# Performance work log

Hardware: AMD Instinct MI355X
Metric: run time of the kernel (lower is better)

## Reference

```python
import jax, jax.numpy as jnp
import numpy as np
import math

EMBED = 8      # forced == n_qubits by the reshape in FeedForwardQuantum
HEADS = 4
DK = EMBED // HEADS
FFN = 2048
EPS = 1e-5


def _layer_norm(x, g, b):
    mu = jnp.mean(x, axis=-1, keepdims=True)
    var = jnp.mean((x - mu) ** 2, axis=-1, keepdims=True)
    return (x - mu) * jax.lax.rsqrt(var + EPS) * g + b


def setup_inputs() -> dict:
    key = jax.random.key(0)
    ks = jax.random.split(key, 8)
    B, S = 8, 2048
    s_e = 1.0 / math.sqrt(EMBED)
    s_q = 1.0 / math.sqrt(EMBED)   # linear1 fan_in = n_qubits = EMBED
    s_f = 1.0 / math.sqrt(FFN)
    return {
        "x": jax.random.normal(ks[0], (B, S, EMBED), dtype=jnp.float32),
        "Wp": jax.random.uniform(ks[1], (EMBED, EMBED), jnp.float32, -s_e, s_e),
        "Wo": jax.random.uniform(ks[2], (EMBED, EMBED), jnp.float32, -s_e, s_e),
        "g1": jnp.ones((EMBED,), jnp.float32),
        "b1": jnp.zeros((EMBED,), jnp.float32),
        "W1": jax.random.uniform(ks[3], (FFN, EMBED), jnp.float32, -s_q, s_q),
        "bb1": jax.random.uniform(ks[4], (FFN,), jnp.float32, -s_q, s_q),
        "W2": jax.random.uniform(ks[5], (EMBED, FFN), jnp.float32, -s_f, s_f),
        "bb2": jax.random.uniform(ks[6], (EMBED,), jnp.float32, -s_f, s_f),
        "g2": jnp.ones((EMBED,), jnp.float32),
        "b2": jnp.zeros((EMBED,), jnp.float32),
    }


def reference(x, Wp, Wo, g1, b1, W1, bb1, W2, bb2, g2, b2):
    B, S, E = x.shape
    # --- multi-head self-attention (q = k = v = proj(x)) ---
    proj = x @ Wp.T                                   # (B,S,E)
    qkv = proj.reshape(B, S, HEADS, DK).transpose(0, 2, 1, 3)  # (B,H,S,dk)
    scores = jnp.einsum("bhqd,bhkd->bhqk", qkv, qkv) / math.sqrt(DK)
    p = jax.nn.softmax(scores, axis=-1)               # (B,H,S,S)
    ctx = jnp.einsum("bhqk,bhkd->bhqd", p, qkv)
    merged = ctx.transpose(0, 2, 1, 3).reshape(B, S, E)
    attn_out = merged @ Wo.T
    x1 = _layer_norm(x + attn_out, g1, b1)
    # --- quantum FFN: RX per wire, CNOT ladder, Z-expectations ---
    # <Z_j> after the circuit = prod_{i<=j} cos(x_i)  (exact closed form)
    out_q = jnp.cumprod(jnp.cos(x1), axis=-1)         # (B,S,n_qubits==E)
    h = jax.nn.relu(out_q @ W1.T + bb1)               # (B,S,FFN)
    ffn_out = h @ W2.T + bb2                          # (B,S,E)
    return _layer_norm(x1 + ffn_out, g2, b2)
```

## Files before the change

kernel.cpp:

```cpp
#include <hip/hip_runtime.h>
#include <math.h>

#define NB   8
#define SEQ  2048
#define EMB  8
#define NH   4
#define NFF  2048
#define NTOK (NB*SEQ)
#define LNEPS 1e-5f

typedef float v2f __attribute__((ext_vector_type(2)));

__device__ __forceinline__ float fexp2(float x) {
#if __has_builtin(__builtin_amdgcn_exp2f)
    return __builtin_amdgcn_exp2f(x);
#else
    return exp2f(x);
#endif
}

__device__ __forceinline__ float dot8(const float4& a, const float4& b,
                                      const float4& c, const float4& d) {
    return a.x*b.x + a.y*b.y + a.z*b.z + a.w*b.w
         + c.x*d.x + c.y*d.y + c.z*d.z + c.w*d.w;
}

__global__ __launch_bounds__(128) void k_prep(const float* __restrict__ x,
                                              const float* __restrict__ Wp,
                                              const float* __restrict__ W2,
                                              float* __restrict__ projH,
                                              float* __restrict__ w2t) {
    int t = blockIdx.x * 128 + threadIdx.x;
    if (t < NTOK) {
        int b = t >> 11, s = t & (SEQ - 1);
        const float4* xr = (const float4*)(x + (size_t)t * EMB);
        float4 xa = xr[0], xb = xr[1];
        float o[8];
#pragma unroll
        for (int e = 0; e < 8; ++e) {
            const float4* wr = (const float4*)(Wp + e * EMB);
            o[e] = dot8(xa, wr[0], xb, wr[1]);
        }
#pragma unroll
        for (int h = 0; h < 4; ++h) {
            *(float2*)(projH + ((size_t)(b * 4 + h) * SEQ + s) * 2) =
                make_float2(o[2 * h], o[2 * h + 1]);
        }
    }
    if (t < NFF) {
        float o[8];
#pragma unroll
        for (int e = 0; e < 8; ++e) o[e] = W2[e * NFF + t];
        float4* wr = (float4*)(w2t + (size_t)t * EMB);
        wr[0] = make_float4(o[0], o[1], o[2], o[3]);
        wr[1] = make_float4(o[4], o[5], o[6], o[7]);
    }
}

#define QCA 64
__global__ __launch_bounds__(256) void k_attn(const float* __restrict__ projH,
                                              float* __restrict__ ctx) {
    __shared__ float Kx[SEQ];
    __shared__ float Ky[SEQ];
    __shared__ float red[3][8][QCA];

    int bid = blockIdx.x;
    int qc  = bid & 31;
    int bh  = bid >> 5;

    const float C   = 1.01001959058f;
    const float RC  = 0.99008003302f;
    const float4* gsr = (const float4*)(projH + (size_t)bh * SEQ * 2);
#pragma unroll
    for (int ii = 0; ii < 4; ++ii) {
        int i = threadIdx.x + 256 * ii;
        float4 v = gsr[i];
        *(float2*)&Kx[2 * i] = make_float2(v.x * C, v.z * C);
        *(float2*)&Ky[2 * i] = make_float2(v.y * C, v.w * C);
    }
    __syncthreads();

    int qg  = threadIdx.x & 31;
    int sub = threadIdx.x >> 5;

    int q0 = qc * QCA + qg * 2;
    float qxa = Kx[q0],     qya = Ky[q0];
    float qxb = Kx[q0 + 1], qyb = Ky[q0 + 1];
    v2f qx2a = {qxa, qxa}, qy2a = {qya, qya};
    v2f qx2b = {qxb, qxb}, qy2b = {qyb, qyb};

    v2f lA = {0.f, 0.f}, axA = {0.f, 0.f}, ayA = {0.f, 0.f};
    v2f lB = {0.f, 0.f}, axB = {0.f, 0.f}, ayB = {0.f, 0.f};

    const float4* Kx4 = (const float4*)Kx;
    const float4* Ky4 = (const float4*)Ky;
    int j04 = sub * 64;
#pragma unroll 2
    for (int jj = 0; jj < 64; ++jj) {
        float4 kx = Kx4[j04 + jj];
        float4 ky = Ky4[j04 + jj];
        v2f k0 = {kx.x, kx.y}, k1 = {kx.z, kx.w};
        v2f m0 = {ky.x, ky.y}, m1 = {ky.z, ky.w};

        v2f s0a = qx2a * k0 + qy2a * m0;
        v2f s1a = qx2a * k1 + qy2a * m1;
        v2f s0b = qx2b * k0 + qy2b * m0;
        v2f s1b = qx2b * k1 + qy2b * m1;

        v2f p0a, p1a, p0b, p1b;
        p0a.x = fexp2(s0a.x); p0a.y = fexp2(s0a.y);
        p1a.x = fexp2(s1a.x); p1a.y = fexp2(s1a.y);
        p0b.x = fexp2(s0b.x); p0b.y = fexp2(s0b.y);
        p1b.x = fexp2(s1b.x); p1b.y = fexp2(s1b.y);

        lA  += p0a;            lB  += p0b;
        axA += p0a * k0;       axB += p0b * k0;
        ayA += p0a * m0;       ayB += p0b * m0;
        lA  += p1a;            lB  += p1b;
        axA += p1a * k1;       axB += p1b * k1;
        ayA += p1a * m1;       ayB += p1b * m1;
    }
    red[0][sub][qg * 2]     = lA.x + lA.y;
    red[1][sub][qg * 2]     = axA.x + axA.y;
    red[2][sub][qg * 2]     = ayA.x + ayA.y;
    red[0][sub][qg * 2 + 1] = lB.x + lB.y;
    red[1][sub][qg * 2 + 1] = axB.x + axB.y;
    red[2][sub][qg * 2 + 1] = ayB.x + ayB.y;
    __syncthreads();

    if (threadIdx.x < QCA) {
        float L = 0.f, A0 = 0.f, A1 = 0.f;
#pragma unroll
        for (int s = 0; s < 8; ++s) {
            L  += red[0][s][threadIdx.x];
            A0 += red[1][s][threadIdx.x];
            A1 += red[2][s][threadIdx.x];
        }
        float inv = RC / L;
        int b = bh >> 2, h = bh & 3;
        int qglob = qc * QCA + threadIdx.x;
        *(float2*)(ctx + ((size_t)b * SEQ + qglob) * EMB + 2 * h) =
            make_float2(A0 * inv, A1 * inv);
    }
}

#define TB3  32
#define FCH3 32
__global__ __launch_bounds__(512) void k_ffn3(const float* __restrict__ ctx,
                                              const float* __restrict__ x,
                                              const float* __restrict__ Wo,
                                              const float* __restrict__ g1,
                                              const float* __restrict__ b1,
                                              const float* __restrict__ W1,
                                              const float* __restrict__ bb1,
                                              const float* __restrict__ w2t,
                                              const float* __restrict__ bb2,
                                              const float* __restrict__ g2,
                                              const float* __restrict__ b2,
                                              float* __restrict__ out) {
    __shared__ float q_lds[TB3][8];
    __shared__ float x1_lds[TB3][8];
    __shared__ float red[8][TB3][8];

    int tid = threadIdx.x;

    if (tid < TB3 * 8) {
        int tl = tid >> 3, e = tid & 7;
        int tok = blockIdx.x * TB3 + tl;
        const float4* cr = (const float4*)(ctx + (size_t)tok * EMB);
        float4 ca = cr[0], cb = cr[1];
        const float4* wr = (const float4*)(Wo + e * EMB);
        float ao = dot8(ca, wr[0], cb, wr[1]);
        float y = x[(size_t)tok * EMB + e] + ao;

        float s8 = y;
        s8 += __shfl_xor(s8, 1);
        s8 += __shfl_xor(s8, 2);
        s8 += __shfl_xor(s8, 4);
        float mu = s8 * 0.125f;
        float d  = y - mu;
        float vs = d * d;
        vs += __shfl_xor(vs, 1);
        vs += __shfl_xor(vs, 2);
        vs += __shfl_xor(vs, 4);
        float r = rsqrtf(vs * 0.125f + LNEPS);
        float v = d * r * g1[e] + b1[e];
        x1_lds[tl][e] = v;

        float p = __cosf(v);
        float t1 = __shfl_up(p, 1, 8); p = (e >= 1) ? p * t1 : p;
        float t2 = __shfl_up(p, 2, 8); p = (e >= 2) ? p * t2 : p;
        float t4 = __shfl_up(p, 4, 8); p = (e >= 4) ? p * t4 : p;
        q_lds[tl][e] = p;
    }
    __syncthreads();

    int tg  = tid & 7;
    int sub = tid >> 3;
    int tl0 = tg * 4;

    float4 qa[4], qb[4];
#pragma unroll
    for (int k = 0; k < 4; ++k) {
        qa[k] = *(const float4*)&q_lds[tl0 + k][0];
        qb[k] = *(const float4*)&q_lds[tl0 + k][4];
    }

    float acc[4][8];
#pragma unroll
    for (int k = 0; k < 4; ++k)
#pragma unroll
        for (int e = 0; e < 8; ++e) acc[k][e] = 0.f;

    int f0 = sub * FCH3;
#pragma unroll 4
    for (int i = 0; i < FCH3; ++i) {
        int f = f0 + i;
        const float4* w1r = (const float4*)(W1 + (size_t)f * EMB);
        float4 wa = w1r[0], wb = w1r[1];
        float bias = bb1[f];
        const float4* w2r = (const float4*)(w2t + (size_t)f * EMB);
        float4 va = w2r[0], vb = w2r[1];
#pragma unroll
        for (int k = 0; k < 4; ++k) {
            float hv = fmaxf(dot8(qa[k], wa, qb[k], wb) + bias, 0.f);
            acc[k][0] = fmaf(hv, va.x, acc[k][0]);
            acc[k][1] = fmaf(hv, va.y, acc[k][1]);
            acc[k][2] = fmaf(hv, va.z, acc[k][2]);
            acc[k][3] = fmaf(hv, va.w, acc[k][3]);
            acc[k][4] = fmaf(hv, vb.x, acc[k][4]);
            acc[k][5] = fmaf(hv, vb.y, acc[k][5]);
            acc[k][6] = fmaf(hv, vb.z, acc[k][6]);
            acc[k][7] = fmaf(hv, vb.w, acc[k][7]);
        }
    }

#pragma unroll
    for (int k = 0; k < 4; ++k)
#pragma unroll
        for (int e = 0; e < 8; ++e) {
            float v = acc[k][e];
            v += __shfl_xor(v, 8);
            v += __shfl_xor(v, 16);
            v += __shfl_xor(v, 32);
            acc[k][e] = v;
        }
    int wv = tid >> 6;
    if (((tid >> 3) & 7) == 0) {
#pragma unroll
        for (int k = 0; k < 4; ++k) {
            float4* d0 = (float4*)&red[wv][tl0 + k][0];
            d0[0] = make_float4(acc[k][0], acc[k][1], acc[k][2], acc[k][3]);
            d0[1] = make_float4(acc[k][4], acc[k][5], acc[k][6], acc[k][7]);
        }
    }
    __syncthreads();

    if (tid < TB3 * 8) {
        int rtok = tid >> 3, re = tid & 7;
        float v = 0.f;
#pragma unroll
        for (int w = 0; w < 8; ++w) v += red[w][rtok][re];
        int tok = blockIdx.x * TB3 + rtok;
        v += bb2[re] + x1_lds[rtok][re];

        float s8 = v;
        s8 += __shfl_xor(s8, 1);
        s8 += __shfl_xor(s8, 2);
        s8 += __shfl_xor(s8, 4);
        float mu = s8 * 0.125f;
        float d  = v - mu;
        float vs = d * d;
        vs += __shfl_xor(vs, 1);
        vs += __shfl_xor(vs, 2);
        vs += __shfl_xor(vs, 4);
        float r = rsqrtf(vs * 0.125f + LNEPS);
        out[(size_t)tok * EMB + re] = d * r * g2[re] + b2[re];
    }
}

extern "C" void kernel_launch(void* const* d_in, const int* in_sizes, int n_in,
                              void* d_out, int out_size, void* d_ws, size_t ws_size,
                              hipStream_t stream) {
    const float* x   = (const float*)d_in[0];
    const float* Wp  = (const float*)d_in[1];
    const float* Wo  = (const float*)d_in[2];
    const float* g1  = (const float*)d_in[3];
    const float* b1  = (const float*)d_in[4];
    const float* W1  = (const float*)d_in[5];
    const float* bb1 = (const float*)d_in[6];
    const float* W2  = (const float*)d_in[7];
    const float* bb2 = (const float*)d_in[8];
    const float* g2  = (const float*)d_in[9];
    const float* b2  = (const float*)d_in[10];
    float* out = (float*)d_out;

    float* ws    = (float*)d_ws;
    float* projH = ws;
    float* ctx   = ws + 131072;
    float* w2t   = ws + 262144;

    hipLaunchKernelGGL(k_prep, dim3(NTOK / 128), dim3(128), 0, stream,
                       x, Wp, W2, projH, w2t);
    hipLaunchKernelGGL(k_attn, dim3((NB * NH) * (SEQ / QCA)), dim3(256), 0, stream,
                       projH, ctx);
    hipLaunchKernelGGL(k_ffn3, dim3(NTOK / TB3), dim3(512), 0, stream,
                       ctx, x, Wo, g1, b1, W1, bb1, w2t, bb2, g2, b2, out);
}
```

Before: 55.50 us.

## Widen per-thread register tiles in attention and FFN kernels

The attention kernel now has each thread handle 4 queries over a 32-chunk key range (16 key slices) instead of 2 queries over 64 chunks. Each K load from LDS is therefore reused across more queries. The FFN kernel doubles its token tile to 64 per block with 8 tokens per thread, reusing each W1/W2 row across more tokens and halving the grid. The cost is more registers per thread, which may lower occupancy, plus a larger reduction over the 16 slices in attention.

```diff
diff --git a/kernel.cpp b/kernel.cpp
--- a/kernel.cpp
+++ b/kernel.cpp
@@ -62,7 +62,7 @@
                                               float* __restrict__ ctx) {
     __shared__ float Kx[SEQ];
     __shared__ float Ky[SEQ];
-    __shared__ float red[3][8][QCA];
+    __shared__ float red[3][16][QCA];
 
     int bid = blockIdx.x;
     int qc  = bid & 31;
@@ -80,58 +80,54 @@
     }
     __syncthreads();
 
-    int qg  = threadIdx.x & 31;
-    int sub = threadIdx.x >> 5;
-
-    int q0 = qc * QCA + qg * 2;
-    float qxa = Kx[q0],     qya = Ky[q0];
-    float qxb = Kx[q0 + 1], qyb = Ky[q0 + 1];
-    v2f qx2a = {qxa, qxa}, qy2a = {qya, qya};
-    v2f qx2b = {qxb, qxb}, qy2b = {qyb, qyb};
-
-    v2f lA = {0.f, 0.f}, axA = {0.f, 0.f}, ayA = {0.f, 0.f};
-    v2f lB = {0.f, 0.f}, axB = {0.f, 0.f}, ayB = {0.f, 0.f};
+    int qg  = threadIdx.x & 15;
+    int sub = threadIdx.x >> 4;
+
+    int q0 = qc * QCA + qg * 4;
+    v2f qx2[4], qy2[4], l[4], ax[4], ay[4];
+#pragma unroll
+    for (int u = 0; u < 4; ++u) {
+        float qx = Kx[q0 + u], qy = Ky[q0 + u];
+        qx2[u] = (v2f){qx, qx};
+        qy2[u] = (v2f){qy, qy};
+        l[u]  = (v2f){0.f, 0.f};
+        ax[u] = (v2f){0.f, 0.f};
+        ay[u] = (v2f){0.f, 0.f};
+    }
 
     const float4* Kx4 = (const float4*)Kx;
     const float4* Ky4 = (const float4*)Ky;
-    int j04 = sub * 64;
+    int j04 = sub * 32;
 #pragma unroll 2
-    for (int jj = 0; jj < 64; ++jj) {
+    for (int jj = 0; jj < 32; ++jj) {
         float4 kx = Kx4[j04 + jj];
         float4 ky = Ky4[j04 + jj];
         v2f k0 = {kx.x, kx.y}, k1 = {kx.z, kx.w};
         v2f m0 = {ky.x, ky.y}, m1 = {ky.z, ky.w};
-
-        v2f s0a = qx2a * k0 + qy2a * m0;
-        v2f s1a = qx2a * k1 + qy2a * m1;
-        v2f s0b = qx2b * k0 + qy2b * m0;
-        v2f s1b = qx2b * k1 + qy2b * m1;
-
-        v2f p0a, p1a, p0b, p1b;
-        p0a.x = fexp2(s0a.x); p0a.y = fexp2(s0a.y);
-        p1a.x = fexp2(s1a.x); p1a.y = fexp2(s1a.y);
-        p0b.x = fexp2(s0b.x); p0b.y = fexp2(s0b.y);
-        p1b.x = fexp2(s1b.x); p1b.y = fexp2(s1b.y);
-
-        lA  += p0a;            lB  += p0b;
-        axA += p0a * k0;       axB += p0b * k0;
-        ayA += p0a * m0;       ayB += p0b * m0;
-        lA  += p1a;            lB  += p1b;
-        axA += p1a * k1;       axB += p1b * k1;
-        ayA += p1a * m1;       ayB += p1b * m1;
-    }
-    red[0][sub][qg * 2]     = lA.x + lA.y;
-    red[1][sub][qg * 2]     = axA.x + axA.y;
-    red[2][sub][qg * 2]     = ayA.x + ayA.y;
-    red[0][sub][qg * 2 + 1] = lB.x + lB.y;
-    red[1][sub][qg * 2 + 1] = axB.x + axB.y;
-    red[2][sub][qg * 2 + 1] = ayB.x + ayB.y;
+#pragma unroll
+        for (int u = 0; u < 4; ++u) {
+            v2f s0 = qx2[u] * k0 + qy2[u] * m0;
+            v2f s1 = qx2[u] * k1 + qy2[u] * m1;
+            v2f p0, p1;
+            p0.x = fexp2(s0.x); p0.y = fexp2(s0.y);
+            p1.x = fexp2(s1.x); p1.y = fexp2(s1.y);
+            l[u]  += p0;        l[u]  += p1;
+            ax[u] += p0 * k0;   ax[u] += p1 * k1;
+            ay[u] += p0 * m0;   ay[u] += p1 * m1;
+        }
+    }
+#pragma unroll
+    for (int u = 0; u < 4; ++u) {
+        red[0][sub][qg * 4 + u] = l[u].x + l[u].y;
+        red[1][sub][qg * 4 + u] = ax[u].x + ax[u].y;
+        red[2][sub][qg * 4 + u] = ay[u].x + ay[u].y;
+    }
     __syncthreads();
 
     if (threadIdx.x < QCA) {
         float L = 0.f, A0 = 0.f, A1 = 0.f;
 #pragma unroll
-        for (int s = 0; s < 8; ++s) {
+        for (int s = 0; s < 16; ++s) {
             L  += red[0][s][threadIdx.x];
             A0 += red[1][s][threadIdx.x];
             A1 += red[2][s][threadIdx.x];
@@ -144,9 +140,9 @@
     }
 }
 
-#define TB3  32
+#define TB3  64
 #define FCH3 32
-__global__ __launch_bounds__(512) void k_ffn3(const float* __restrict__ ctx,
+__global__ __launch_bounds__(512) void k_ffn5(const float* __restrict__ ctx,
                                               const float* __restrict__ x,
                                               const float* __restrict__ Wo,
                                               const float* __restrict__ g1,
@@ -164,7 +160,7 @@
 
     int tid = threadIdx.x;
 
-    if (tid < TB3 * 8) {
+    {
         int tl = tid >> 3, e = tid & 7;
         int tok = blockIdx.x * TB3 + tl;
         const float4* cr = (const float4*)(ctx + (size_t)tok * EMB);
@@ -195,25 +191,26 @@
     }
     __syncthreads();
 
-    int tg  = tid & 7;
-    int sub = tid >> 3;
-    int tl0 = tg * 4;
-
-    float4 qa[4], qb[4];
-#pragma unroll
-    for (int k = 0; k < 4; ++k) {
+    int tg    = tid & 7;
+    int fslot = (tid >> 3) & 7;
+    int wv    = tid >> 6;
+    int tl0   = tg * 8;
+
+    float4 qa[8], qb[8];
+#pragma unroll
+    for (int k = 0; k < 8; ++k) {
         qa[k] = *(const float4*)&q_lds[tl0 + k][0];
         qb[k] = *(const float4*)&q_lds[tl0 + k][4];
     }
 
-    float acc[4][8];
-#pragma unroll
-    for (int k = 0; k < 4; ++k)
+    float acc[8][8];
+#pragma unroll
+    for (int k = 0; k < 8; ++k)
 #pragma unroll
         for (int e = 0; e < 8; ++e) acc[k][e] = 0.f;
 
-    int f0 = sub * FCH3;
-#pragma unroll 4
+    int f0 = (wv * 8 + fslot) * FCH3;
+#pragma unroll 2
     for (int i = 0; i < FCH3; ++i) {
         int f = f0 + i;
         const float4* w1r = (const float4*)(W1 + (size_t)f * EMB);
@@ -222,7 +219,7 @@
         const float4* w2r = (const float4*)(w2t + (size_t)f * EMB);
         float4 va = w2r[0], vb = w2r[1];
 #pragma unroll
-        for (int k = 0; k < 4; ++k) {
+        for (int k = 0; k < 8; ++k) {
             float hv = fmaxf(dot8(qa[k], wa, qb[k], wb) + bias, 0.f);
             acc[k][0] = fmaf(hv, va.x, acc[k][0]);
             acc[k][1] = fmaf(hv, va.y, acc[k][1]);
@@ -236,7 +233,7 @@
     }
 
 #pragma unroll
-    for (int k = 0; k < 4; ++k)
+    for (int k = 0; k < 8; ++k)
 #pragma unroll
         for (int e = 0; e < 8; ++e) {
             float v = acc[k][e];
@@ -245,10 +242,9 @@
             v += __shfl_xor(v, 32);
             acc[k][e] = v;
         }
-    int wv = tid >> 6;
-    if (((tid >> 3) & 7) == 0) {
-#pragma unroll
-        for (int k = 0; k < 4; ++k) {
+    if (fslot == 0) {
+#pragma unroll
+        for (int k = 0; k < 8; ++k) {
             float4* d0 = (float4*)&red[wv][tl0 + k][0];
             d0[0] = make_float4(acc[k][0], acc[k][1], acc[k][2], acc[k][3]);
             d0[1] = make_float4(acc[k][4], acc[k][5], acc[k][6], acc[k][7]);
@@ -256,7 +252,7 @@
     }
     __syncthreads();
 
-    if (tid < TB3 * 8) {
+    {
         int rtok = tid >> 3, re = tid & 7;
         float v = 0.f;
 #pragma unroll
@@ -304,6 +300,6 @@
                        x, Wp, W2, projH, w2t);
     hipLaunchKernelGGL(k_attn, dim3((NB * NH) * (SEQ / QCA)), dim3(256), 0, stream,
                        projH, ctx);
-    hipLaunchKernelGGL(k_ffn3, dim3(NTOK / TB3), dim3(512), 0, stream,
+    hipLaunchKernelGGL(k_ffn5, dim3(NTOK / TB3), dim3(512), 0, stream,
                        ctx, x, Wo, g1, b1, W1, bb1, w2t, bb2, g2, b2, out);
 }
```

After: 53.94 us. -2.8%, faster.
